# Kernel optimization log

Hardware: AMD Instinct MI355X
Metric: run time of the kernel (lower is better)

The kernel has to match this reference:

```python
import jax, jax.numpy as jnp
import numpy as np


def setup_inputs() -> dict:
    key = jax.random.key(0)
    k1, k2, k3 = jax.random.split(key, 3)
    x = jax.random.normal(k1, (1, 512, 14, 14), dtype=jnp.float32)
    w1 = jax.random.normal(k2, (16, 64, 3), dtype=jnp.float32)
    w2 = jax.random.normal(k3, (32, 8, 3), dtype=jnp.float32)
    return {"x": x, "w1": w1, "w2": w2}


def reference(x, w1, w2):
    SHIFT = 1  # module picks +/-1 at random init; fixed to +1
    H = W = 14
    # reshape (1,512,14,14) -> (1, i=64, o=8, H, W), roll along H
    xr = x.reshape(1, 64, 8, H, W)
    xr = jnp.roll(xr, SHIFT, axis=3)
    # unfold with kernel (3,1), pad (1,0) along H == stack 3 shifted slices
    xp = jnp.pad(xr, ((0, 0), (0, 0), (0, 0), (1, 1), (0, 0)))
    t3 = jnp.stack([xp[:, :, :, j:j + H, :] for j in range(3)], axis=3)  # (1,64,8,3,14,14)
    # conv 1: contract i=64 channels and j=3 taps per group o -> k=16 outputs
    t4 = jnp.einsum('liojmn,kij->lkomn', t3, w1)  # (1,16,8,14,14)
    # unfold with kernel (3,1), pad (1,0) along W (after the (1,1792,14,1) reshape)
    tp = jnp.pad(t4, ((0, 0), (0, 0), (0, 0), (0, 0), (1, 1)))
    t5 = jnp.stack([tp[..., k:k + W] for k in range(3)], axis=4)  # (1,16,8,14,3,14)
    # conv 2: contract j=8 group channels and k=3 taps -> i=32 outputs per o=16
    t6 = jnp.einsum('lojmkn,ijk->liomn', t5, w2)  # (1,32,16,14,14)
    return t6.reshape(1, 512, H, W)
```

## Files before the change

### kernel.cpp

```cpp
#include <hip/hip_runtime.h>


__global__ __launch_bounds__(512) void fused_shift_conv(
    const float* __restrict__ x,
    const float* __restrict__ w1,
    const float* __restrict__ w2,
    float* __restrict__ out)
{
    const int bx = blockIdx.x;
    const int m  = bx >> 4;
    const int o2 = bx & 15;
    const int t  = threadIdx.x;

    __shared__ float w1s[64 * 3];
    __shared__ float w2s[32 * 8 * 3];
    __shared__ float t4p[4][112];
    __shared__ float t4s[112];

    if (t < 192) w1s[t] = w1[o2 * 192 + t];
    if (t >= 256 && t < 256 + 192) {
        ((float4*)w2s)[t - 256] = ((const float4*)w2)[t - 256];
    }
    __syncthreads();

    if (t < 448) {
        const int quarter = t / 112;
        const int r = t % 112;
        const int o = r / 14;
        const int n = r % 14;
        const int ibase = quarter * 16;
        float acc = 0.f;
        #pragma unroll
        for (int j = 0; j < 3; ++j) {
            const int hp = m + j - 1;
            if (hp >= 0 && hp < 14) {
                const int row = (hp + 13) % 14;
                const float* xp = x + (size_t)(ibase * 8 + o) * 196 + row * 14 + n;
                const float* wp = w1s + ibase * 3 + j;
                #pragma unroll
                for (int i = 0; i < 16; ++i) {
                    acc += xp[(size_t)i * 8 * 196] * wp[i * 3];
                }
            }
        }
        t4p[quarter][r] = acc;
    }
    __syncthreads();
    if (t < 112) t4s[t] = (t4p[0][t] + t4p[1][t]) + (t4p[2][t] + t4p[3][t]);
    __syncthreads();

    if (t < 448) {
        const int n  = t % 14;
        const int i2 = t / 14;
        const float* wp = w2s + i2 * 24;
        float acc = 0.f;
        #pragma unroll
        for (int j = 0; j < 8; ++j) {
            const float* tp = t4s + j * 14;
            #pragma unroll
            for (int k = 0; k < 3; ++k) {
                const int nn = n + k - 1;
                if (nn >= 0 && nn < 14) acc += tp[nn] * wp[j * 3 + k];
            }
        }
        out[((size_t)(i2 * 16 + o2) * 14 + m) * 14 + n] = acc;
    }
}

extern "C" void kernel_launch(void* const* d_in, const int* in_sizes, int n_in,
                              void* d_out, int out_size, void* d_ws, size_t ws_size,
                              hipStream_t stream) {
    const float* x  = (const float*)d_in[0];
    const float* w1 = (const float*)d_in[1];
    const float* w2 = (const float*)d_in[2];
    float* out = (float*)d_out;
    fused_shift_conv<<<dim3(224), dim3(512), 0, stream>>>(x, w1, w2, out);
}
```

Before: 60.79 us.

## Restructure conv1 stage: float2 loads, register weights, shuffle reduction, fewer barriers

The first convolution stage now has 224 threads, each computing two adjacent output columns with float2 loads of x. The w1 weights are loaded straight into registers as float4 instead of staged in shared memory. All x loads are issued before the FMAs to raise memory-level parallelism. The four-way partial-sum reduction now uses wavefront shuffles instead of a shared-memory buffer, which removes two barriers. The w2 copy into shared memory overlaps with this work on otherwise idle threads. In exchange, per-thread register use rises and fewer threads issue loads.

```diff
diff --git a/kernel.cpp b/kernel.cpp
--- a/kernel.cpp
+++ b/kernel.cpp
@@ -12,41 +12,60 @@
     const int o2 = bx & 15;
     const int t  = threadIdx.x;
 
-    __shared__ float w1s[64 * 3];
     __shared__ float w2s[32 * 8 * 3];
-    __shared__ float t4p[4][112];
     __shared__ float t4s[112];
 
-    if (t < 192) w1s[t] = w1[o2 * 192 + t];
-    if (t >= 256 && t < 256 + 192) {
-        ((float4*)w2s)[t - 256] = ((const float4*)w2)[t - 256];
-    }
-    __syncthreads();
+    if (t < 224) {
+        const int quarter = t & 3;
+        const int r  = t >> 2;
+        const int o  = r / 7;
+        const int n0 = (r % 7) * 2;
+        const int ibase = quarter * 16;
 
-    if (t < 448) {
-        const int quarter = t / 112;
-        const int r = t % 112;
-        const int o = r / 14;
-        const int n = r % 14;
-        const int ibase = quarter * 16;
-        float acc = 0.f;
+        float4 w1v[12];
+        {
+            const float4* w1p = (const float4*)(w1 + (size_t)o2 * 192 + ibase * 3);
+            #pragma unroll
+            for (int q = 0; q < 12; ++q) w1v[q] = w1p[q];
+        }
+
+        float2 xv[3][16];
         #pragma unroll
         for (int j = 0; j < 3; ++j) {
             const int hp = m + j - 1;
             if (hp >= 0 && hp < 14) {
                 const int row = (hp + 13) % 14;
-                const float* xp = x + (size_t)(ibase * 8 + o) * 196 + row * 14 + n;
-                const float* wp = w1s + ibase * 3 + j;
+                const float* xp = x + (size_t)(ibase * 8 + o) * 196 + row * 14 + n0;
                 #pragma unroll
-                for (int i = 0; i < 16; ++i) {
-                    acc += xp[(size_t)i * 8 * 196] * wp[i * 3];
-                }
+                for (int i = 0; i < 16; ++i)
+                    xv[j][i] = *(const float2*)(xp + (size_t)i * 8 * 196);
+            } else {
+                #pragma unroll
+                for (int i = 0; i < 16; ++i) xv[j][i] = make_float2(0.f, 0.f);
             }
         }
-        t4p[quarter][r] = acc;
+
+        float2 acc = make_float2(0.f, 0.f);
+        const float* w1f = (const float*)w1v;
+        #pragma unroll
+        for (int j = 0; j < 3; ++j) {
+            #pragma unroll
+            for (int i = 0; i < 16; ++i) {
+                const float w = w1f[i * 3 + j];
+                acc.x += xv[j][i].x * w;
+                acc.y += xv[j][i].y * w;
+            }
+        }
+
+        acc.x += __shfl_xor(acc.x, 1);
+        acc.y += __shfl_xor(acc.y, 1);
+        acc.x += __shfl_xor(acc.x, 2);
+        acc.y += __shfl_xor(acc.y, 2);
+        if (quarter == 0) *(float2*)(t4s + o * 14 + n0) = acc;
+    } else if (t >= 320) {
+        ((float4*)w2s)[t - 320] = ((const float4*)w2)[t - 320];
     }
-    __syncthreads();
-    if (t < 112) t4s[t] = (t4p[0][t] + t4p[1][t]) + (t4p[2][t] + t4p[3][t]);
+
     __syncthreads();
 
     if (t < 448) {
```

Result: slower. 63.51 us (+4.5%).
